# Kernel optimization log

Hardware: AMD Instinct MI355X
Metric: run time of the kernel (lower is better)

The kernel has to match this reference:

```python
import jax, jax.numpy as jnp
import numpy as np

B, T, C, HS = 512, 256, 384, 64  # batch, block_size, n_embed, head_size


def setup_inputs() -> dict:
    key = jax.random.key(0)
    kx, kq, kk, kv = jax.random.split(key, 4)
    x = jax.random.normal(kx, (B, T, C), dtype=jnp.float32)
    # Linear(n_embed, head_size, bias=False) weights stored as [in, out]
    s = 1.0 / np.sqrt(C)
    Wq = jax.random.normal(kq, (C, HS), dtype=jnp.float32) * s
    Wk = jax.random.normal(kk, (C, HS), dtype=jnp.float32) * s
    Wv = jax.random.normal(kv, (C, HS), dtype=jnp.float32) * s
    return {"x": x, "Wq": Wq, "Wk": Wk, "Wv": Wv}


def reference(x, Wq, Wk, Wv):
    Bb, Tt, Cc = x.shape
    q = jnp.einsum('btc,ch->bth', x, Wq)
    k = jnp.einsum('btc,ch->bth', x, Wk)
    v = jnp.einsum('btc,ch->bth', x, Wv)
    # NOTE: original scales by C**-0.5 (embed dim), NOT head_size**-0.5
    wei = jnp.einsum('bqh,bkh->bqk', q, k) * (Cc ** -0.5)
    # causal mask: tril == 0 (strict upper triangle) -> -inf
    causal = jnp.tril(jnp.ones((Tt, Tt), dtype=bool))
    wei = jnp.where(causal[None, :, :], wei, -jnp.inf)
    # NOTE: original applies softmax over dim=1 (query axis) — replicated faithfully
    wei = jax.nn.softmax(wei, axis=1)
    out = jnp.einsum('bqk,bkh->bqh', wei, v)
    return out
```

## Files before the change

### kernel.cpp

```cpp
#include <hip/hip_runtime.h>

typedef float  f32x4  __attribute__((ext_vector_type(4)));
typedef __bf16 bf16x8 __attribute__((ext_vector_type(8)));

#define CC 384

__device__ __forceinline__ unsigned short f2bf(float f) {
  union { float f; unsigned int u; } x; x.f = f;
  unsigned int u = x.u;
  return (unsigned short)((u + 0x7fffu + ((u >> 16) & 1u)) >> 16);
}

__device__ __forceinline__ f32x4 mfma16(bf16x8 a, bf16x8 b, f32x4 c) {
  return __builtin_amdgcn_mfma_f32_16x16x32_bf16(a, b, c, 0, 0, 0);
}

__global__ void repack_w(const float* __restrict__ Wq, const float* __restrict__ Wk,
                         const float* __restrict__ Wv, unsigned short* __restrict__ wf) {
  int e = blockIdx.x * 512 + threadIdx.x;
  int k = e / 192;
  int n = e - k * 192;
  const float* W = (n < 64) ? Wq : (n < 128) ? Wk : Wv;
  float val = W[k * 64 + (n & 63)];
  int kk = k >> 5;
  int lane = (((k >> 3) & 3) << 4) | (n & 15);
  int j = k & 7;
  int nt = n >> 4;
  wf[(size_t)(((kk * 12 + nt) << 6) + lane) * 8 + j] = f2bf(val);
}

__global__ __launch_bounds__(512, 1) void fused(const float* __restrict__ x,
                                                const unsigned short* __restrict__ wf,
                                                float* __restrict__ out) {
  __shared__ __attribute__((aligned(16))) unsigned char smem[119808];
  unsigned short (*Sx)[72] = (unsigned short(*)[72])smem;
  unsigned short (*kL)[72] = (unsigned short(*)[72])(smem + 36864);
  unsigned short (*vT)[264] = (unsigned short(*)[264])(smem + 73728);
  float* pm = (float*)(smem + 107520);
  float* ps = pm + 1024;
  float* gg = ps + 1024;
  unsigned short* wst = (unsigned short*)smem;

  const int tid = threadIdx.x;
  const int w = tid >> 6, lane = tid & 63;
  const int l15 = lane & 15, lhi = lane >> 4;
  const int b = blockIdx.x;
  const int mts[2] = {w, 15 - w};

  const float* xr0 = x + ((size_t)b * 256 + mts[0] * 16 + l15) * CC + lhi * 8;
  const float* xr1 = x + ((size_t)b * 256 + mts[1] * 16 + l15) * CC + lhi * 8;

  f32x4 zero = {0.f, 0.f, 0.f, 0.f};
  f32x4 acc[2][12];
#pragma unroll
  for (int i = 0; i < 2; ++i)
#pragma unroll
    for (int nt = 0; nt < 12; ++nt) acc[i][nt] = zero;

#define STAGE(kp_, b_) do {                                                                           \
    const unsigned short* s_ = wf + (size_t)(kp_) * 6144 + tid * 8;                                   \
    unsigned short* d_ = wst + (b_) * 6144 + tid * 8;                                                 \
    __builtin_amdgcn_global_load_lds((const __attribute__((address_space(1))) void*)(s_),             \
                                     (__attribute__((address_space(3))) void*)(d_), 16, 0, 0);        \
    if (tid < 256)                                                                                    \
      __builtin_amdgcn_global_load_lds((const __attribute__((address_space(1))) void*)(s_ + 4096),    \
                                       (__attribute__((address_space(3))) void*)(d_ + 4096), 16, 0, 0);\
  } while (0)

  STAGE(0, 0);
  f32x4 aC[2][2];
  aC[0][0] = *(const f32x4*)(xr0);     aC[0][1] = *(const f32x4*)(xr0 + 4);
  aC[1][0] = *(const f32x4*)(xr1);     aC[1][1] = *(const f32x4*)(xr1 + 4);

  for (int kp = 0; kp < 12; ++kp) {
    __syncthreads();
    f32x4 aN[2][2];
#pragma unroll
    for (int i = 0; i < 2; ++i) { aN[i][0] = zero; aN[i][1] = zero; }
    if (kp < 11) {
      const int o = (kp + 1) * 32;
      aN[0][0] = *(const f32x4*)(xr0 + o);     aN[0][1] = *(const f32x4*)(xr0 + o + 4);
      aN[1][0] = *(const f32x4*)(xr1 + o);     aN[1][1] = *(const f32x4*)(xr1 + o + 4);
      STAGE(kp + 1, (kp + 1) & 1);
    }
    const bf16x8* bp = (const bf16x8*)(wst + (kp & 1) * 6144) + lane;
#pragma unroll
    for (int i = 0; i < 2; ++i) {
      bf16x8 af;
#pragma unroll
      for (int j = 0; j < 4; ++j) { af[j] = (__bf16)aC[i][0][j]; af[4 + j] = (__bf16)aC[i][1][j]; }
#pragma unroll
      for (int nt = 0; nt < 12; ++nt) acc[i][nt] = mfma16(af, bp[nt * 64], acc[i][nt]);
    }
#pragma unroll
    for (int i = 0; i < 2; ++i) { aC[i][0] = aN[i][0]; aC[i][1] = aN[i][1]; }
  }
#undef STAGE
  __syncthreads();

  const float qs = 0.05103103630798288f;
#pragma unroll
  for (int i = 0; i < 2; ++i) {
    const int rb = mts[i] * 16 + lhi * 4;
#pragma unroll
    for (int nt = 0; nt < 4; ++nt) {
      const int h = nt * 16 + l15;
#pragma unroll
      for (int r = 0; r < 4; ++r) Sx[rb + r][h] = f2bf(acc[i][nt][r] * qs);
    }
#pragma unroll
    for (int nt = 4; nt < 8; ++nt) {
      const int h = (nt - 4) * 16 + l15;
#pragma unroll
      for (int r = 0; r < 4; ++r) kL[rb + r][h] = f2bf(acc[i][nt][r]);
    }
#pragma unroll
    for (int nt = 8; nt < 12; ++nt) {
      const int h = (nt - 8) * 16 + l15;
      unsigned long long pk =
          (unsigned long long)f2bf(acc[i][nt][0]) |
          ((unsigned long long)f2bf(acc[i][nt][1]) << 16) |
          ((unsigned long long)f2bf(acc[i][nt][2]) << 32) |
          ((unsigned long long)f2bf(acc[i][nt][3]) << 48);
      *(unsigned long long*)&vT[h][rb] = pk;
    }
  }
  __syncthreads();

  bf16x8 qf[2][2];
#pragma unroll
  for (int i = 0; i < 2; ++i)
#pragma unroll
    for (int kk = 0; kk < 2; ++kk)
      qf[i][kk] = *(const bf16x8*)&Sx[mts[i] * 16 + l15][kk * 32 + lhi * 8];

  f32x4 oacc[2][4];
#pragma unroll
  for (int i = 0; i < 2; ++i)
#pragma unroll
    for (int nh = 0; nh < 4; ++nh) oacc[i][nh] = zero;

  for (int p = 0; p < 4; ++p) {
    const int p4 = 4 * p;
    const bool any = (mts[1] >= p4);
    if (any) {
      bf16x8 kf[4][2];
#pragma unroll
      for (int c = 0; c < 4; ++c)
#pragma unroll
        for (int kk = 0; kk < 2; ++kk)
          kf[c][kk] = *(const bf16x8*)&kL[p * 64 + c * 16 + l15][kk * 32 + lhi * 8];
#pragma unroll
      for (int i = 0; i < 2; ++i) {
        const int mt = mts[i];
        if (mt < p4) continue;
        const int cmax = mt - p4;
        const int rowb = mt * 16 + lhi * 4;
#pragma unroll
        for (int c = 0; c < 4; ++c) {
          const int cs = c * 16 + l15;
          if (c <= cmax) {
            f32x4 s = zero;
            s = mfma16(qf[i][0], kf[c][0], s);
            s = mfma16(qf[i][1], kf[c][1], s);
            const int cg = p * 64 + cs;
            const bool v0 = (rowb + 0) >= cg, v1 = (rowb + 1) >= cg;
            const bool v2 = (rowb + 2) >= cg, v3 = (rowb + 3) >= cg;
            float m = -1e30f;
            m = fmaxf(m, v0 ? s[0] : -1e30f);
            m = fmaxf(m, v1 ? s[1] : -1e30f);
            m = fmaxf(m, v2 ? s[2] : -1e30f);
            m = fmaxf(m, v3 ? s[3] : -1e30f);
            m = fmaxf(m, __shfl_xor(m, 16));
            m = fmaxf(m, __shfl_xor(m, 32));
            const float e0 = v0 ? __expf(s[0] - m) : 0.f;
            const float e1 = v1 ? __expf(s[1] - m) : 0.f;
            const float e2 = v2 ? __expf(s[2] - m) : 0.f;
            const float e3 = v3 ? __expf(s[3] - m) : 0.f;
            float t = e0 + e1 + e2 + e3;
            t += __shfl_xor(t, 16);
            t += __shfl_xor(t, 32);
            Sx[rowb + 0][cs] = f2bf(e0);
            Sx[rowb + 1][cs] = f2bf(e1);
            Sx[rowb + 2][cs] = f2bf(e2);
            Sx[rowb + 3][cs] = f2bf(e3);
            if (lhi == 0) { pm[mt * 64 + cs] = m; ps[mt * 64 + cs] = t; }
          } else {
            if (lhi == 0) { pm[mt * 64 + cs] = -1e30f; ps[mt * 64 + cs] = 0.f; }
          }
        }
      }
    }
    __syncthreads();
    {
      float M = -1e30f;
      for (int mt = p4; mt < 16; ++mt) M = fmaxf(M, pm[mt * 64 + lane]);
      float L = 0.f;
      for (int mt = p4; mt < 16; ++mt) L += ps[mt * 64 + lane] * __expf(pm[mt * 64 + lane] - M);
      const float rv = 1.0f / L;
      int mtw = p4 + w;
      if (mtw < 16) gg[mtw * 64 + lane] = __expf(pm[mtw * 64 + lane] - M) * rv;
      mtw += 8;
      if (mtw < 16) gg[mtw * 64 + lane] = __expf(pm[mtw * 64 + lane] - M) * rv;
    }
    __syncthreads();
    if (any) {
      bf16x8 vf[4][2];
#pragma unroll
      for (int nh = 0; nh < 4; ++nh)
#pragma unroll
        for (int kk = 0; kk < 2; ++kk)
          vf[nh][kk] = *(const bf16x8*)&vT[nh * 16 + l15][p * 64 + kk * 32 + lhi * 8];
#pragma unroll
      for (int i = 0; i < 2; ++i) {
        const int mt = mts[i];
        if (mt < p4) continue;
        const int grow = mt * 16 + l15;
        const int dmax = mt - p4;
#pragma unroll
        for (int kk = 0; kk < 2; ++kk) {
          if (kk == 1 && dmax <= 1) continue;
          const int c0 = kk * 32 + lhi * 8;
          bf16x8 se = *(const bf16x8*)&Sx[grow][c0];
          f32x4 gA = *(const f32x4*)&gg[mt * 64 + c0];
          f32x4 gB = *(const f32x4*)&gg[mt * 64 + c0 + 4];
          const int cg0 = p * 64 + c0;
          bf16x8 wfr;
#pragma unroll
          for (int j = 0; j < 4; ++j)
            wfr[j] = (cg0 + j <= grow) ? (__bf16)((float)se[j] * gA[j]) : (__bf16)0.f;
#pragma unroll
          for (int j = 0; j < 4; ++j)
            wfr[4 + j] = (cg0 + 4 + j <= grow) ? (__bf16)((float)se[4 + j] * gB[j]) : (__bf16)0.f;
#pragma unroll
          for (int nh = 0; nh < 4; ++nh) oacc[i][nh] = mfma16(wfr, vf[nh][kk], oacc[i][nh]);
        }
      }
    }
  }
#pragma unroll
  for (int i = 0; i < 2; ++i) {
    const int rb = mts[i] * 16 + lhi * 4;
#pragma unroll
    for (int nh = 0; nh < 4; ++nh) {
      const int h = nh * 16 + l15;
#pragma unroll
      for (int r = 0; r < 4; ++r)
        out[(size_t)b * 16384 + (size_t)(rb + r) * 64 + h] = oacc[i][nh][r];
    }
  }
}

extern "C" void kernel_launch(void* const* d_in, const int* in_sizes, int n_in,
                              void* d_out, int out_size, void* d_ws, size_t ws_size,
                              hipStream_t stream) {
  const float* x  = (const float*)d_in[0];
  const float* Wq = (const float*)d_in[1];
  const float* Wk = (const float*)d_in[2];
  const float* Wv = (const float*)d_in[3];
  float* out = (float*)d_out;

  unsigned short* wf = (unsigned short*)d_ws;

  repack_w<<<144, 512, 0, stream>>>(Wq, Wk, Wv, wf);
  fused<<<512, 512, 0, stream>>>(x, wf, out);
}
```

Before: 82.87 us.

## Load projection weights directly into registers instead of LDS staging

The QKV projection loop stops staging the packed bf16 weights through double-buffered LDS with async global-to-LDS loads and per-iteration barriers. Each wave now reads its weight fragments straight from global memory into a register double buffer, and the loop is fully unrolled. Launch bounds are also raised to request two blocks per CU. This removes the 12 __syncthreads and the LDS traffic, at the cost of many more VGPRs (24 bf16x8 of weights) and every wave fetching the full weight set redundantly through the cache. With roughly 117KB of static LDS per block a second block probably cannot be resident, so the launch-bounds change may mostly just force register limits and risk spills.

```diff
diff --git a/kernel.cpp b/kernel.cpp
--- a/kernel.cpp
+++ b/kernel.cpp
@@ -29,7 +29,7 @@
   wf[(size_t)(((kk * 12 + nt) << 6) + lane) * 8 + j] = f2bf(val);
 }
 
-__global__ __launch_bounds__(512, 1) void fused(const float* __restrict__ x,
+__global__ __launch_bounds__(512, 2) void fused(const float* __restrict__ x,
                                                 const unsigned short* __restrict__ wf,
                                                 float* __restrict__ out) {
   __shared__ __attribute__((aligned(16))) unsigned char smem[119808];
@@ -39,7 +39,6 @@
   float* pm = (float*)(smem + 107520);
   float* ps = pm + 1024;
   float* gg = ps + 1024;
-  unsigned short* wst = (unsigned short*)smem;
 
   const int tid = threadIdx.x;
   const int w = tid >> 6, lane = tid & 63;
@@ -49,6 +48,7 @@
 
   const float* xr0 = x + ((size_t)b * 256 + mts[0] * 16 + l15) * CC + lhi * 8;
   const float* xr1 = x + ((size_t)b * 256 + mts[1] * 16 + l15) * CC + lhi * 8;
+  const unsigned short* wl = wf + lane * 8;
 
   f32x4 zero = {0.f, 0.f, 0.f, 0.f};
   f32x4 acc[2][12];
@@ -57,46 +57,44 @@
 #pragma unroll
     for (int nt = 0; nt < 12; ++nt) acc[i][nt] = zero;
 
-#define STAGE(kp_, b_) do {                                                                           \
-    const unsigned short* s_ = wf + (size_t)(kp_) * 6144 + tid * 8;                                   \
-    unsigned short* d_ = wst + (b_) * 6144 + tid * 8;                                                 \
-    __builtin_amdgcn_global_load_lds((const __attribute__((address_space(1))) void*)(s_),             \
-                                     (__attribute__((address_space(3))) void*)(d_), 16, 0, 0);        \
-    if (tid < 256)                                                                                    \
-      __builtin_amdgcn_global_load_lds((const __attribute__((address_space(1))) void*)(s_ + 4096),    \
-                                       (__attribute__((address_space(3))) void*)(d_ + 4096), 16, 0, 0);\
+  {
+    bf16x8 wreg[2][12];
+    f32x4  xreg[2][4];
+
+#define LOADW(kp_, s_) do {                                                     \
+    _Pragma("unroll")                                                           \
+    for (int nt_ = 0; nt_ < 12; ++nt_)                                          \
+      wreg[s_][nt_] = *(const bf16x8*)(wl + ((kp_) * 12 + nt_) * 512);          \
   } while (0)
-
-  STAGE(0, 0);
-  f32x4 aC[2][2];
-  aC[0][0] = *(const f32x4*)(xr0);     aC[0][1] = *(const f32x4*)(xr0 + 4);
-  aC[1][0] = *(const f32x4*)(xr1);     aC[1][1] = *(const f32x4*)(xr1 + 4);
-
-  for (int kp = 0; kp < 12; ++kp) {
-    __syncthreads();
-    f32x4 aN[2][2];
-#pragma unroll
-    for (int i = 0; i < 2; ++i) { aN[i][0] = zero; aN[i][1] = zero; }
-    if (kp < 11) {
-      const int o = (kp + 1) * 32;
-      aN[0][0] = *(const f32x4*)(xr0 + o);     aN[0][1] = *(const f32x4*)(xr0 + o + 4);
-      aN[1][0] = *(const f32x4*)(xr1 + o);     aN[1][1] = *(const f32x4*)(xr1 + o + 4);
-      STAGE(kp + 1, (kp + 1) & 1);
-    }
-    const bf16x8* bp = (const bf16x8*)(wst + (kp & 1) * 6144) + lane;
-#pragma unroll
-    for (int i = 0; i < 2; ++i) {
-      bf16x8 af;
-#pragma unroll
-      for (int j = 0; j < 4; ++j) { af[j] = (__bf16)aC[i][0][j]; af[4 + j] = (__bf16)aC[i][1][j]; }
-#pragma unroll
-      for (int nt = 0; nt < 12; ++nt) acc[i][nt] = mfma16(af, bp[nt * 64], acc[i][nt]);
-    }
-#pragma unroll
-    for (int i = 0; i < 2; ++i) { aC[i][0] = aN[i][0]; aC[i][1] = aN[i][1]; }
-  }
-#undef STAGE
-  __syncthreads();
+#define LOADX(kp_, s_) do {                                                     \
+    const int o_ = (kp_) * 32;                                                  \
+    xreg[s_][0] = *(const f32x4*)(xr0 + o_);                                    \
+    xreg[s_][1] = *(const f32x4*)(xr0 + o_ + 4);                                \
+    xreg[s_][2] = *(const f32x4*)(xr1 + o_);                                    \
+    xreg[s_][3] = *(const f32x4*)(xr1 + o_ + 4);                                \
+  } while (0)
+
+    LOADW(0, 0);
+    LOADX(0, 0);
+#pragma unroll
+    for (int kp = 0; kp < 12; ++kp) {
+      const int cur = kp & 1, nxt = cur ^ 1;
+      if (kp < 11) { LOADW(kp + 1, nxt); LOADX(kp + 1, nxt); }
+#pragma unroll
+      for (int i = 0; i < 2; ++i) {
+        bf16x8 af;
+#pragma unroll
+        for (int j = 0; j < 4; ++j) {
+          af[j]     = (__bf16)xreg[cur][2 * i][j];
+          af[4 + j] = (__bf16)xreg[cur][2 * i + 1][j];
+        }
+#pragma unroll
+        for (int nt = 0; nt < 12; ++nt) acc[i][nt] = mfma16(af, wreg[cur][nt], acc[i][nt]);
+      }
+    }
+#undef LOADW
+#undef LOADX
+  }
 
   const float qs = 0.05103103630798288f;
 #pragma unroll
```

New measurement: 90.57 us. 1.09x slower.

## Double-buffer score tile to overlap next QK softmax with current PV

Applied to the files above, without the earlier changes.

Splits the attention loop into S (QK^T plus local softmax) and PV phases, and double-buffers the probability tile in shared memory. The next block's S phase can then run right after the current PV, dropping one barrier per iteration and letting MFMA work from both phases interleave. This grows shared memory to about 153 KB. It also changes launch bounds to request 2 blocks per CU, which tightens the register budget and may cause spills, even though the larger LDS footprint likely still allows only one block per CU.

```diff
diff --git a/kernel.cpp b/kernel.cpp
--- a/kernel.cpp
+++ b/kernel.cpp
@@ -4,6 +4,8 @@
 typedef __bf16 bf16x8 __attribute__((ext_vector_type(8)));
 
 #define CC 384
+#define AS1 __attribute__((address_space(1)))
+#define AS3 __attribute__((address_space(3)))
 
 __device__ __forceinline__ unsigned short f2bf(float f) {
   union { float f; unsigned int u; } x; x.f = f;
@@ -29,14 +31,15 @@
   wf[(size_t)(((kk * 12 + nt) << 6) + lane) * 8 + j] = f2bf(val);
 }
 
-__global__ __launch_bounds__(512, 1) void fused(const float* __restrict__ x,
+__global__ __launch_bounds__(512, 2) void fused(const float* __restrict__ x,
                                                 const unsigned short* __restrict__ wf,
                                                 float* __restrict__ out) {
-  __shared__ __attribute__((aligned(16))) unsigned char smem[119808];
-  unsigned short (*Sx)[72] = (unsigned short(*)[72])smem;
-  unsigned short (*kL)[72] = (unsigned short(*)[72])(smem + 36864);
-  unsigned short (*vT)[264] = (unsigned short(*)[264])(smem + 73728);
-  float* pm = (float*)(smem + 107520);
+  __shared__ __attribute__((aligned(16))) unsigned char smem[156672];
+  __bf16 (*Sx0)[72] = (__bf16(*)[72])smem;
+  __bf16 (*Sx1)[72] = (__bf16(*)[72])(smem + 36864);
+  unsigned short (*kL)[72] = (unsigned short(*)[72])(smem + 73728);
+  unsigned short (*vT)[264] = (unsigned short(*)[264])(smem + 110592);
+  float* pm = (float*)(smem + 144384);
   float* ps = pm + 1024;
   float* gg = ps + 1024;
   unsigned short* wst = (unsigned short*)smem;
@@ -57,14 +60,13 @@
 #pragma unroll
     for (int nt = 0; nt < 12; ++nt) acc[i][nt] = zero;
 
-#define STAGE(kp_, b_) do {                                                                           \
-    const unsigned short* s_ = wf + (size_t)(kp_) * 6144 + tid * 8;                                   \
-    unsigned short* d_ = wst + (b_) * 6144 + tid * 8;                                                 \
-    __builtin_amdgcn_global_load_lds((const __attribute__((address_space(1))) void*)(s_),             \
-                                     (__attribute__((address_space(3))) void*)(d_), 16, 0, 0);        \
-    if (tid < 256)                                                                                    \
-      __builtin_amdgcn_global_load_lds((const __attribute__((address_space(1))) void*)(s_ + 4096),    \
-                                       (__attribute__((address_space(3))) void*)(d_ + 4096), 16, 0, 0);\
+#define STAGE(kp_, b_) do {                                                                   \
+    const unsigned short* s_ = wf + (size_t)(kp_) * 6144 + tid * 8;                           \
+    unsigned short* d_ = wst + (b_) * 6144 + tid * 8;                                         \
+    __builtin_amdgcn_global_load_lds((const AS1 void*)(s_), (AS3 void*)(d_), 16, 0, 0);       \
+    if (tid < 256)                                                                            \
+      __builtin_amdgcn_global_load_lds((const AS1 void*)(s_ + 4096), (AS3 void*)(d_ + 4096),  \
+                                       16, 0, 0);                                             \
   } while (0)
 
   STAGE(0, 0);
@@ -106,7 +108,8 @@
     for (int nt = 0; nt < 4; ++nt) {
       const int h = nt * 16 + l15;
 #pragma unroll
-      for (int r = 0; r < 4; ++r) Sx[rb + r][h] = f2bf(acc[i][nt][r] * qs);
+      for (int r = 0; r < 4; ++r)
+        *(unsigned short*)&Sx0[rb + r][h] = f2bf(acc[i][nt][r] * qs);
     }
 #pragma unroll
     for (int nt = 4; nt < 8; ++nt) {
@@ -132,7 +135,7 @@
   for (int i = 0; i < 2; ++i)
 #pragma unroll
     for (int kk = 0; kk < 2; ++kk)
-      qf[i][kk] = *(const bf16x8*)&Sx[mts[i] * 16 + l15][kk * 32 + lhi * 8];
+      qf[i][kk] = *(const bf16x8*)&Sx0[mts[i] * 16 + l15][kk * 32 + lhi * 8];
 
   f32x4 oacc[2][4];
 #pragma unroll
@@ -140,58 +143,97 @@
 #pragma unroll
     for (int nh = 0; nh < 4; ++nh) oacc[i][nh] = zero;
 
+  auto do_S = [&](int sp, __bf16 (*SxW)[72]) {
+    const int p4 = 4 * sp;
+    if (mts[1] < p4) return;
+    bf16x8 kf[4][2];
+#pragma unroll
+    for (int c = 0; c < 4; ++c)
+#pragma unroll
+      for (int kk = 0; kk < 2; ++kk)
+        kf[c][kk] = *(const bf16x8*)&kL[sp * 64 + c * 16 + l15][kk * 32 + lhi * 8];
+#pragma unroll
+    for (int i = 0; i < 2; ++i) {
+      const int mt = mts[i];
+      if (mt < p4) continue;
+      const int cmax = mt - p4;
+      const int rowb = mt * 16 + lhi * 4;
+#pragma unroll
+      for (int c = 0; c < 4; ++c) {
+        const int cs = c * 16 + l15;
+        if (c <= cmax) {
+          f32x4 s = zero;
+          s = mfma16(qf[i][0], kf[c][0], s);
+          s = mfma16(qf[i][1], kf[c][1], s);
+          const int cg = sp * 64 + cs;
+          const bool v0 = (rowb + 0) >= cg, v1 = (rowb + 1) >= cg;
+          const bool v2 = (rowb + 2) >= cg, v3 = (rowb + 3) >= cg;
+          float m = -1e30f;
+          m = fmaxf(m, v0 ? s[0] : -1e30f);
+          m = fmaxf(m, v1 ? s[1] : -1e30f);
+          m = fmaxf(m, v2 ? s[2] : -1e30f);
+          m = fmaxf(m, v3 ? s[3] : -1e30f);
+          m = fmaxf(m, __shfl_xor(m, 16));
+          m = fmaxf(m, __shfl_xor(m, 32));
+          const float e0 = v0 ? __expf(s[0] - m) : 0.f;
+          const float e1 = v1 ? __expf(s[1] - m) : 0.f;
+          const float e2 = v2 ? __expf(s[2] - m) : 0.f;
+          const float e3 = v3 ? __expf(s[3] - m) : 0.f;
+          float t = e0 + e1 + e2 + e3;
+          t += __shfl_xor(t, 16);
+          t += __shfl_xor(t, 32);
+          SxW[rowb + 0][cs] = (__bf16)e0;
+          SxW[rowb + 1][cs] = (__bf16)e1;
+          SxW[rowb + 2][cs] = (__bf16)e2;
+          SxW[rowb + 3][cs] = (__bf16)e3;
+          if (lhi == 0) { pm[mt * 64 + cs] = m; ps[mt * 64 + cs] = t; }
+        } else {
+          if (lhi == 0) { pm[mt * 64 + cs] = -1e30f; ps[mt * 64 + cs] = 0.f; }
+        }
+      }
+    }
+  };
+
+  auto do_PV = [&](int sp, const __bf16 (*SxR)[72]) {
+    const int p4 = 4 * sp;
+    if (mts[1] < p4) return;
+    bf16x8 vf[4][2];
+#pragma unroll
+    for (int nh = 0; nh < 4; ++nh)
+#pragma unroll
+      for (int kk = 0; kk < 2; ++kk)
+        vf[nh][kk] = *(const bf16x8*)&vT[nh * 16 + l15][sp * 64 + kk * 32 + lhi * 8];
+#pragma unroll
+    for (int i = 0; i < 2; ++i) {
+      const int mt = mts[i];
+      if (mt < p4) continue;
+      const int grow = mt * 16 + l15;
+      const int dmax = mt - p4;
+#pragma unroll
+      for (int kk = 0; kk < 2; ++kk) {
+        if (kk == 1 && dmax <= 1) continue;
+        const int c0 = kk * 32 + lhi * 8;
+        bf16x8 se = *(const bf16x8*)&SxR[grow][c0];
+        f32x4 gA = *(const f32x4*)&gg[mt * 64 + c0];
+        f32x4 gB = *(const f32x4*)&gg[mt * 64 + c0 + 4];
+        const int cg0 = sp * 64 + c0;
+        bf16x8 wfr;
+#pragma unroll
+        for (int j = 0; j < 4; ++j)
+          wfr[j] = (cg0 + j <= grow) ? (__bf16)((float)se[j] * gA[j]) : (__bf16)0.f;
+#pragma unroll
+        for (int j = 0; j < 4; ++j)
+          wfr[4 + j] = (cg0 + 4 + j <= grow) ? (__bf16)((float)se[4 + j] * gB[j]) : (__bf16)0.f;
+#pragma unroll
+        for (int nh = 0; nh < 4; ++nh) oacc[i][nh] = mfma16(wfr, vf[nh][kk], oacc[i][nh]);
+      }
+    }
+  };
+
+  do_S(0, Sx0);
+  __syncthreads();
   for (int p = 0; p < 4; ++p) {
     const int p4 = 4 * p;
-    const bool any = (mts[1] >= p4);
-    if (any) {
-      bf16x8 kf[4][2];
-#pragma unroll
-      for (int c = 0; c < 4; ++c)
-#pragma unroll
-        for (int kk = 0; kk < 2; ++kk)
-          kf[c][kk] = *(const bf16x8*)&kL[p * 64 + c * 16 + l15][kk * 32 + lhi * 8];
-#pragma unroll
-      for (int i = 0; i < 2; ++i) {
-        const int mt = mts[i];
-        if (mt < p4) continue;
-        const int cmax = mt - p4;
-        const int rowb = mt * 16 + lhi * 4;
-#pragma unroll
-        for (int c = 0; c < 4; ++c) {
-          const int cs = c * 16 + l15;
-          if (c <= cmax) {
-            f32x4 s = zero;
-            s = mfma16(qf[i][0], kf[c][0], s);
-            s = mfma16(qf[i][1], kf[c][1], s);
-            const int cg = p * 64 + cs;
-            const bool v0 = (rowb + 0) >= cg, v1 = (rowb + 1) >= cg;
-            const bool v2 = (rowb + 2) >= cg, v3 = (rowb + 3) >= cg;
-            float m = -1e30f;
-            m = fmaxf(m, v0 ? s[0] : -1e30f);
-            m = fmaxf(m, v1 ? s[1] : -1e30f);
-            m = fmaxf(m, v2 ? s[2] : -1e30f);
-            m = fmaxf(m, v3 ? s[3] : -1e30f);
-            m = fmaxf(m, __shfl_xor(m, 16));
-            m = fmaxf(m, __shfl_xor(m, 32));
-            const float e0 = v0 ? __expf(s[0] - m) : 0.f;
-            const float e1 = v1 ? __expf(s[1] - m) : 0.f;
-            const float e2 = v2 ? __expf(s[2] - m) : 0.f;
-            const float e3 = v3 ? __expf(s[3] - m) : 0.f;
-            float t = e0 + e1 + e2 + e3;
-            t += __shfl_xor(t, 16);
-            t += __shfl_xor(t, 32);
-            Sx[rowb + 0][cs] = f2bf(e0);
-            Sx[rowb + 1][cs] = f2bf(e1);
-            Sx[rowb + 2][cs] = f2bf(e2);
-            Sx[rowb + 3][cs] = f2bf(e3);
-            if (lhi == 0) { pm[mt * 64 + cs] = m; ps[mt * 64 + cs] = t; }
-          } else {
-            if (lhi == 0) { pm[mt * 64 + cs] = -1e30f; ps[mt * 64 + cs] = 0.f; }
-          }
-        }
-      }
-    }
-    __syncthreads();
     {
       float M = -1e30f;
       for (int mt = p4; mt < 16; ++mt) M = fmaxf(M, pm[mt * 64 + lane]);
@@ -204,38 +246,10 @@
       if (mtw < 16) gg[mtw * 64 + lane] = __expf(pm[mtw * 64 + lane] - M) * rv;
     }
     __syncthreads();
-    if (any) {
-      bf16x8 vf[4][2];
-#pragma unroll
-      for (int nh = 0; nh < 4; ++nh)
-#pragma unroll
-        for (int kk = 0; kk < 2; ++kk)
-          vf[nh][kk] = *(const bf16x8*)&vT[nh * 16 + l15][p * 64 + kk * 32 + lhi * 8];
-#pragma unroll
-      for (int i = 0; i < 2; ++i) {
-        const int mt = mts[i];
-        if (mt < p4) continue;
-        const int grow = mt * 16 + l15;
-        const int dmax = mt - p4;
-#pragma unroll
-        for (int kk = 0; kk < 2; ++kk) {
-          if (kk == 1 && dmax <= 1) continue;
-          const int c0 = kk * 32 + lhi * 8;
-          bf16x8 se = *(const bf16x8*)&Sx[grow][c0];
-          f32x4 gA = *(const f32x4*)&gg[mt * 64 + c0];
-          f32x4 gB = *(const f32x4*)&gg[mt * 64 + c0 + 4];
-          const int cg0 = p * 64 + c0;
-          bf16x8 wfr;
-#pragma unroll
-          for (int j = 0; j < 4; ++j)
-            wfr[j] = (cg0 + j <= grow) ? (__bf16)((float)se[j] * gA[j]) : (__bf16)0.f;
-#pragma unroll
-          for (int j = 0; j < 4; ++j)
-            wfr[4 + j] = (cg0 + 4 + j <= grow) ? (__bf16)((float)se[4 + j] * gB[j]) : (__bf16)0.f;
-#pragma unroll
-          for (int nh = 0; nh < 4; ++nh) oacc[i][nh] = mfma16(wfr, vf[nh][kk], oacc[i][nh]);
-        }
-      }
+    do_PV(p, (p & 1) ? (const __bf16(*)[72])Sx1 : (const __bf16(*)[72])Sx0);
+    if (p < 3) {
+      do_S(p + 1, (p & 1) ? Sx0 : Sx1);
+      __syncthreads();
     }
   }
 #pragma unroll
```

Measured after the change: 85.41 us. 1.03x slower.
